# Kernel optimization log

Hardware: AMD Instinct MI355X
Metric: run time of the kernel (lower is better)

Reference implementation:

```python
import jax, jax.numpy as jnp
import numpy as np

N, G, F, H, P, OUT = 100000, 64, 64, 128, 2, 2
E = 1_600_000
BN_EPS = 1e-5  # PyG BatchNorm eps; eval mode with running_mean=0, running_var=1


def setup_inputs() -> dict:
    key = jax.random.key(0)
    ks = iter(jax.random.split(key, 64))

    def lin(din, dout):
        w = jax.random.normal(next(ks), (din, dout), jnp.float32) / np.sqrt(din).astype(np.float32)
        return w, jnp.zeros((dout,), jnp.float32)

    inp = {}
    inp["x"] = jax.random.normal(next(ks), (N, F), jnp.float32)
    inp["pos"] = jax.random.normal(next(ks), (N, P), jnp.float32)
    inp["edge_index"] = jax.random.randint(next(ks), (2, E), 0, N, dtype=jnp.int64) if jax.config.jax_enable_x64 else jax.random.randint(next(ks), (2, E), 0, N)
    inp["batch"] = jnp.sort(jax.random.randint(next(ks), (N,), 0, G))
    dims = [F + P, H + P, H + P]
    for l, din in enumerate(dims):
        w1, b1 = lin(din, H)
        w2, b2 = lin(H, H)
        inp[f"w{l}1"], inp[f"b{l}1"] = w1, b1
        inp[f"g{l}1"], inp[f"be{l}1"] = jnp.ones((H,), jnp.float32), jnp.zeros((H,), jnp.float32)
        inp[f"w{l}2"], inp[f"b{l}2"] = w2, b2
        inp[f"g{l}2"], inp[f"be{l}2"] = jnp.ones((H,), jnp.float32), jnp.zeros((H,), jnp.float32)
    inp["wlin"], inp["blin"] = lin(H, OUT)
    return inp


def _bn(h, g, b):
    # eval-mode BatchNorm with running_mean=0, running_var=1
    return h * (g * (1.0 / np.sqrt(1.0 + BN_EPS)).astype(np.float32)) + b


def _mlp(h, w1, b1, g1, be1, w2, b2, g2, be2):
    h = jax.nn.relu(_bn(h @ w1 + b1, g1, be1))
    return jax.nn.relu(_bn(h @ w2 + b2, g2, be2))


def _gin_max(x, src, dst, mlp_params):
    # GINConv with aggr='max', eps=0: mlp(x + max_{j in N(i)} x_j), empty neighborhoods -> 0 (PyG scatter fill)
    agg = jax.ops.segment_max(x[src], dst, num_segments=N)  # [N, C]
    agg = jnp.where(jnp.isneginf(agg), jnp.zeros((), agg.dtype), agg)
    return _mlp(x + agg, *mlp_params)


def reference(x, pos, edge_index, batch,
              w01, b01, g01, be01, w02, b02, g02, be02,
              w11, b11, g11, be11, w12, b12, g12, be12,
              w21, b21, g21, be21, w22, b22, g22, be22,
              wlin, blin):
    src, dst = edge_index[0], edge_index[1]
    h = jnp.concatenate([x, pos], axis=-1)                        # [N, F+P]
    h = _gin_max(h, src, dst, (w01, b01, g01, be01, w02, b02, g02, be02))
    h = jnp.concatenate([h, pos], axis=-1)                        # [N, H+P]
    h = _gin_max(h, src, dst, (w11, b11, g11, be11, w12, b12, g12, be12))
    h = jnp.concatenate([h, pos], axis=-1)
    h = _gin_max(h, src, dst, (w21, b21, g21, be21, w22, b22, g22, be22))
    pooled = jax.ops.segment_max(h, batch, num_segments=G)        # global_max_pool -> [G, H]
    pooled = jnp.where(jnp.isneginf(pooled), jnp.zeros((), pooled.dtype), pooled)
    return pooled @ wlin + blin                                   # logits [G, OUT]
```

## Files before the change

kernel.cpp:

```cpp
#include <hip/hip_runtime.h>
#include <hip/hip_fp16.h>
#include <math.h>
#include <string.h>

constexpr int HDIM = 128;
constexpr int RB   = 136;
constexpr int ZS   = 168;
constexpr float BN_INV = 0.99999500003749980f;

typedef _Float16 half8v __attribute__((ext_vector_type(8)));
typedef __attribute__((ext_vector_type(4))) float float4v;

__device__ __forceinline__ unsigned pkmax(unsigned a, unsigned b) {
  unsigned r;
  asm volatile("v_pk_max_f16 %0, %1, %2" : "=v"(r) : "v"(a), "v"(b));
  return r;
}
__device__ __forceinline__ unsigned pkadd(unsigned a, unsigned b) {
  unsigned r;
  asm volatile("v_pk_add_f16 %0, %1, %2" : "=v"(r) : "v"(a), "v"(b));
  return r;
}

__device__ __forceinline__ float us2f(unsigned short u) { __half h; memcpy(&h, &u, 2); return __half2float(h); }
__device__ __forceinline__ unsigned short f2us(float f) {
  __half h = __float2half(f); unsigned short u; memcpy(&u, &h, 2); return u;
}

__device__ __forceinline__ unsigned encf(float f) {
  unsigned u = __float_as_uint(f);
  return (u & 0x80000000u) ? ~u : (u | 0x80000000u);
}
__device__ __forceinline__ float decf(unsigned u) {
  return (u & 0x80000000u) ? __uint_as_float(u ^ 0x80000000u) : __uint_as_float(~u);
}

__global__ __launch_bounds__(256) void k_bscan(
    const int* __restrict__ bcnt, int* __restrict__ bbase, int* __restrict__ gcur,
    int nbkt, int E) {
  __shared__ int s[256];
  int tid = threadIdx.x;
  int v = (tid < nbkt) ? bcnt[tid] : 0;
  s[tid] = v;
  __syncthreads();
  for (int off = 1; off < 256; off <<= 1) {
    int t = (tid >= off) ? s[tid - off] : 0;
    __syncthreads();
    s[tid] += t;
    __syncthreads();
  }
  if (tid < nbkt) {
    int e = s[tid] - v;
    bbase[tid] = e;
    gcur[tid] = e;
  }
  if (tid == 0) bbase[nbkt] = E;
}

__global__ __launch_bounds__(256) void k_bscatter(
    const int* __restrict__ ei, int* __restrict__ gcur,
    unsigned long long* __restrict__ sorted, int E, int shift, int nbkt) {
  __shared__ int hcnt[256];
  __shared__ int hstart[256];
  __shared__ int gbase[256];
  __shared__ unsigned long long sbuf[4096];

  const int tid = threadIdx.x;
  const int base = blockIdx.x * 4096;
  const int validCount = min(4096, E - base);

  hcnt[tid] = 0;
  __syncthreads();

  int sArr[16], dArr[16];
#pragma unroll
  for (int k = 0; k < 16; ++k) {
    int e = base + k * 256 + tid;
    if (e < E) {
      sArr[k] = ei[e];
      dArr[k] = ei[E + e];
      atomicAdd(&hcnt[dArr[k] >> shift], 1);
    } else {
      sArr[k] = -1; dArr[k] = -1;
    }
  }
  __syncthreads();

  {
    int v = hcnt[tid];
    __shared__ int sc[256];
    sc[tid] = v;
    __syncthreads();
    for (int off = 1; off < 256; off <<= 1) {
      int t = (tid >= off) ? sc[tid - off] : 0;
      __syncthreads();
      sc[tid] += t;
      __syncthreads();
    }
    hstart[tid] = sc[tid] - v;
    if (tid < nbkt && v > 0) gbase[tid] = atomicAdd(&gcur[tid], v);
    hcnt[tid] = sc[tid] - v;
  }
  __syncthreads();

#pragma unroll
  for (int k = 0; k < 16; ++k) {
    if (dArr[k] >= 0) {
      int b = dArr[k] >> shift;
      int p = atomicAdd(&hcnt[b], 1);
      sbuf[p] = ((unsigned long long)(unsigned)dArr[k] << 32) | (unsigned)sArr[k];
    }
  }
  __syncthreads();

  for (int p = tid; p < validCount; p += 256) {
    unsigned long long v = sbuf[p];
    int b = (int)(v >> 32) >> shift;
    sorted[(size_t)gbase[b] + (p - hstart[b])] = v;
  }
}

__global__ __launch_bounds__(256) void k_bcsr(
    const unsigned long long* __restrict__ sorted, const int* __restrict__ bbase,
    int* __restrict__ rowptr, int* __restrict__ eidx,
    int shift, int nbkt, int N, int E) {
  __shared__ int cnt[512];
  __shared__ int excl[512];
  __shared__ int sc[256];
  const int b = blockIdx.x, tid = threadIdx.x;
  const int nodeBase = b << shift;
  const int nodesHere = min(512, N - nodeBase);
  const int lo = bbase[b], hi = bbase[b + 1];

  cnt[tid] = 0; cnt[tid + 256] = 0;
  __syncthreads();
  for (int i = lo + tid; i < hi; i += 256) {
    int d = (int)(sorted[i] >> 32);
    atomicAdd(&cnt[d - nodeBase], 1);
  }
  __syncthreads();
  int a0 = cnt[2 * tid], a1 = cnt[2 * tid + 1];
  int pv = a0 + a1;
  sc[tid] = pv;
  __syncthreads();
  for (int off = 1; off < 256; off <<= 1) {
    int t = (tid >= off) ? sc[tid - off] : 0;
    __syncthreads();
    sc[tid] += t;
    __syncthreads();
  }
  int pe = sc[tid] - pv;
  excl[2 * tid] = pe;
  excl[2 * tid + 1] = pe + a0;
  __syncthreads();
  for (int i = tid; i < 512; i += 256) {
    if (i < nodesHere) rowptr[nodeBase + i] = lo + excl[i];
    cnt[i] = excl[i];
  }
  if (b == nbkt - 1 && tid == 0) rowptr[N] = E;
  __syncthreads();
  for (int i = lo + tid; i < hi; i += 256) {
    unsigned long long v = sorted[i];
    int d = (int)(v >> 32);
    int s = (int)(v & 0xFFFFFFFFu);
    int p = atomicAdd(&cnt[d - nodeBase], 1);
    eidx[lo + p] = s;
  }
}

struct PrepArgs {
  const float *x, *pos;
  const float *w01, *w11, *w21, *w02, *w12, *w22;
  const float *b01, *g01, *e01, *b02, *g02, *e02;
  const float *b11, *g11, *e11, *b12, *g12, *e12;
  const float *b21, *g21, *e21, *b22, *g22, *e22;
  const int *ei;
  int *bcnt;
  unsigned short *h0;
  unsigned short *Wt;
  unsigned *pooled;
  float *Ep;
  int N, GH, E, shift, nbkt, chunks;
};

__global__ __launch_bounds__(256) void k_prep(PrepArgs a) {
  __shared__ int hb[256];
  const int tid = threadIdx.x;
  const int gtid = blockIdx.x * 256 + tid;

  if (blockIdx.x < a.chunks) {
    hb[tid] = 0;
    __syncthreads();
    const int base = blockIdx.x * 4096;
#pragma unroll
    for (int k = 0; k < 16; ++k) {
      int e = base + k * 256 + tid;
      if (e < a.E) atomicAdd(&hb[a.ei[a.E + e] >> a.shift], 1);
    }
    __syncthreads();
    if (tid < a.nbkt && hb[tid] > 0) atomicAdd(&a.bcnt[tid], hb[tid]);
  }

  if (gtid < a.GH) a.pooled[gtid] = 0x007FFFFFu;

  if (gtid < 61440) {
    int l = gtid / 20480, rem = gtid % 20480;
    int n = rem / 160, k = rem % 160;
    const float* W = (l == 0) ? a.w01 : ((l == 1) ? a.w11 : a.w21);
    int K = (l == 0) ? 66 : 130;
    float v = (k < K) ? W[(size_t)k * 128 + n] : 0.0f;
    a.Wt[gtid] = f2us(v);
  } else if (gtid < 110592) {
    int idx2 = gtid - 61440;
    int l = idx2 / 16384, rem = idx2 % 16384;
    int n = rem / 128, k = rem % 128;
    const float* W = (l == 0) ? a.w02 : ((l == 1) ? a.w12 : a.w22);
    a.Wt[gtid] = f2us(W[(size_t)k * 128 + n]);
  } else if (gtid < 110592 + 768) {
    int idx = gtid - 110592;
    int col = idx & 127, stage = (idx >> 7) & 1, l = idx >> 8;
    const float *bb, *gg, *ee;
    if (l == 0)      { if (!stage) { bb = a.b01; gg = a.g01; ee = a.e01; } else { bb = a.b02; gg = a.g02; ee = a.e02; } }
    else if (l == 1) { if (!stage) { bb = a.b11; gg = a.g11; ee = a.e11; } else { bb = a.b12; gg = a.g12; ee = a.e12; } }
    else             { if (!stage) { bb = a.b21; gg = a.g21; ee = a.e21; } else { bb = a.b22; gg = a.g22; ee = a.e22; } }
    float s = gg[col] * BN_INV;
    a.Ep[l * 512 + stage * 256 + col] = s;
    a.Ep[l * 512 + stage * 256 + 128 + col] = bb[col] * s + ee[col];
  }

  int r = gtid >> 6;
  if (r < a.N) {
    int lane = gtid & 63;
    a.h0[(size_t)r * RB + lane] = f2us(a.x[(size_t)r * 64 + lane]);
    float pv = (lane < 2) ? a.pos[(size_t)r * 2 + lane] : 0.0f;
    a.h0[(size_t)r * RB + 64 + lane] = f2us(pv);
    if (lane < 8) {
      a.h0[(size_t)r * RB + 128 + lane] = f2us((lane < 2) ? a.pos[(size_t)r * 2 + lane] : 0.0f);
    }
  }
}

__global__ __launch_bounds__(256) void k_agg(
    const unsigned short* __restrict__ hcat, const int* __restrict__ rowptr,
    const int* __restrict__ eidx, unsigned short* __restrict__ z,
    int actA, int doTail, int N) {
  int wid = (int)((blockIdx.x * 256 + threadIdx.x) >> 6);
  if (wid >= N) return;
  const int lane = threadIdx.x & 63;
  const int half = lane >> 5;
  const int lc = lane & 31;
  const bool act = (lc < actA) || (doTail && lc == 16);
  const int cb = lc * 8;

  const unsigned NEGINF = 0xFC00FC00u;
  unsigned m0 = NEGINF, m1 = NEGINF, m2 = NEGINF, m3 = NEGINF;

  int r0 = rowptr[wid], r1 = rowptr[wid + 1];
  int e = r0 + half;
  for (; e + 6 < r1; e += 8) {
    int s0 = eidx[e], s1 = eidx[e + 2], s2 = eidx[e + 4], s3 = eidx[e + 6];
    if (act) {
      uint4 v0 = *(const uint4*)(hcat + (size_t)s0 * RB + cb);
      uint4 v1 = *(const uint4*)(hcat + (size_t)s1 * RB + cb);
      uint4 v2 = *(const uint4*)(hcat + (size_t)s2 * RB + cb);
      uint4 v3 = *(const uint4*)(hcat + (size_t)s3 * RB + cb);
      m0 = pkmax(m0, pkmax(pkmax(v0.x, v1.x), pkmax(v2.x, v3.x)));
      m1 = pkmax(m1, pkmax(pkmax(v0.y, v1.y), pkmax(v2.y, v3.y)));
      m2 = pkmax(m2, pkmax(pkmax(v0.z, v1.z), pkmax(v2.z, v3.z)));
      m3 = pkmax(m3, pkmax(pkmax(v0.w, v1.w), pkmax(v2.w, v3.w)));
    }
  }
  for (; e < r1; e += 2) {
    int s = eidx[e];
    if (act) {
      uint4 va = *(const uint4*)(hcat + (size_t)s * RB + cb);
      m0 = pkmax(m0, va.x);
      m1 = pkmax(m1, va.y);
      m2 = pkmax(m2, va.z);
      m3 = pkmax(m3, va.w);
    }
  }

  m0 = pkmax(m0, (unsigned)__shfl_xor((int)m0, 32));
  m1 = pkmax(m1, (unsigned)__shfl_xor((int)m1, 32));
  m2 = pkmax(m2, (unsigned)__shfl_xor((int)m2, 32));
  m3 = pkmax(m3, (unsigned)__shfl_xor((int)m3, 32));

  if (half == 0 && act) {
    if (r0 == r1) { m0 = 0u; m1 = 0u; m2 = 0u; m3 = 0u; }
    uint4 sv = *(const uint4*)(hcat + (size_t)wid * RB + cb);
    uint4 o;
    o.x = pkadd(sv.x, m0);
    o.y = pkadd(sv.y, m1);
    o.z = pkadd(sv.z, m2);
    o.w = pkadd(sv.w, m3);
    *(uint4*)(z + (size_t)wid * RB + cb) = o;
  }
}

__global__ __launch_bounds__(256) void k_mlp(
    const unsigned short* __restrict__ z, int kc1, int ntot, int nreal,
    const unsigned short* __restrict__ Wt1, const float* __restrict__ Ep1,
    const unsigned short* __restrict__ Wt2, const float* __restrict__ Ep2,
    unsigned short* __restrict__ out, int N) {
  __shared__ __align__(16) unsigned short zs[4][16][ZS];
  const int tid = threadIdx.x;
  const int w = tid >> 6, lane = tid & 63;
  const int arow = lane & 15;
  const int grp  = lane >> 4;
  const int row0 = blockIdx.x * 64 + w * 16;

  for (int c = lane; c < 16 * ntot; c += 64) {
    int r = c / ntot, seg = c - r * ntot;
    uint4 v = make_uint4(0u, 0u, 0u, 0u);
    if (seg < nreal) {
      int gr = row0 + r;
      if (gr >= N) gr = N - 1;
      v = *(const uint4*)(z + (size_t)gr * RB + seg * 8);
    }
    *(uint4*)(&zs[w][r][seg * 8]) = v;
  }

  float4v acc[8];
#pragma unroll
  for (int i = 0; i < 8; ++i) acc[i] = (float4v){0.f, 0.f, 0.f, 0.f};

  for (int kc = 0; kc < kc1; ++kc) {
    half8v a = *(const half8v*)(&zs[w][arow][kc * 32 + grp * 8]);
    const unsigned short* wp = Wt1 + (size_t)arow * 160 + kc * 32 + grp * 8;
#pragma unroll
    for (int nt = 0; nt < 8; ++nt) {
      half8v b = *(const half8v*)(wp + (size_t)(nt * 16) * 160);
      acc[nt] = __builtin_amdgcn_mfma_f32_16x16x32_f16(a, b, acc[nt], 0, 0, 0);
    }
  }

#pragma unroll
  for (int nt = 0; nt < 8; ++nt) {
    int col = nt * 16 + arow;
    float sc = Ep1[col];
    float cc = Ep1[128 + col];
#pragma unroll
    for (int j = 0; j < 4; ++j) {
      float v = fmaxf(fmaf(acc[nt][j], sc, cc), 0.0f);
      zs[w][grp * 4 + j][col] = f2us(v);
    }
  }

#pragma unroll
  for (int i = 0; i < 8; ++i) acc[i] = (float4v){0.f, 0.f, 0.f, 0.f};
  for (int kc = 0; kc < 4; ++kc) {
    half8v a = *(const half8v*)(&zs[w][arow][kc * 32 + grp * 8]);
    const unsigned short* wp = Wt2 + (size_t)arow * HDIM + kc * 32 + grp * 8;
#pragma unroll
    for (int nt = 0; nt < 8; ++nt) {
      half8v b = *(const half8v*)(wp + (size_t)(nt * 16) * HDIM);
      acc[nt] = __builtin_amdgcn_mfma_f32_16x16x32_f16(a, b, acc[nt], 0, 0, 0);
    }
  }

#pragma unroll
  for (int nt = 0; nt < 8; ++nt) {
    int col = nt * 16 + arow;
    float sc = Ep2[col];
    float cc = Ep2[128 + col];
#pragma unroll
    for (int j = 0; j < 4; ++j) {
      float v = fmaxf(fmaf(acc[nt][j], sc, cc), 0.0f);
      zs[w][grp * 4 + j][col] = f2us(v);
    }
  }
  for (int c = lane; c < 16 * 16; c += 64) {
    int r = c >> 4, seg = c & 15;
    int gr = row0 + r;
    if (gr < N) {
      *(uint4*)(out + (size_t)gr * RB + seg * 8) = *(const uint4*)(&zs[w][r][seg * 8]);
    }
  }
}

__global__ __launch_bounds__(128) void k_pool(
    const unsigned short* __restrict__ hcat, const int* __restrict__ batch,
    unsigned* __restrict__ pooled, int N) {
  int base = blockIdx.x * 128;
  int c = threadIdx.x;
  int end = min(base + 128, N);
  int curg = -1;
  float m = -INFINITY;
  for (int i = base; i < end; ++i) {
    int g = batch[i];
    if (g != curg) {
      if (curg >= 0) atomicMax(&pooled[curg * HDIM + c], encf(m));
      curg = g;
      m = -INFINITY;
    }
    m = fmaxf(m, us2f(hcat[(size_t)i * RB + c]));
  }
  if (curg >= 0) atomicMax(&pooled[curg * HDIM + c], encf(m));
}

__global__ __launch_bounds__(64) void k_final(
    const unsigned* __restrict__ pooled, const float* __restrict__ wlin,
    const float* __restrict__ blin, float* __restrict__ out) {
  int g = blockIdx.x;
  int lane = threadIdx.x;
  float v0 = decf(pooled[g * HDIM + lane]);
  float v1 = decf(pooled[g * HDIM + 64 + lane]);
  if (v0 == -INFINITY) v0 = 0.0f;
  if (v1 == -INFINITY) v1 = 0.0f;
  float p0 = v0 * wlin[lane * 2 + 0] + v1 * wlin[(64 + lane) * 2 + 0];
  float p1 = v0 * wlin[lane * 2 + 1] + v1 * wlin[(64 + lane) * 2 + 1];
  for (int off = 32; off > 0; off >>= 1) {
    p0 += __shfl_down(p0, off);
    p1 += __shfl_down(p1, off);
  }
  if (lane == 0) {
    out[g * 2 + 0] = p0 + blin[0];
    out[g * 2 + 1] = p1 + blin[1];
  }
}

static inline size_t ws_align(size_t x) { return (x + 511) & ~(size_t)511; }

extern "C" void kernel_launch(void* const* d_in, const int* in_sizes, int n_in,
                              void* d_out, int out_size, void* d_ws, size_t ws_size,
                              hipStream_t stream) {
  const float* x     = (const float*)d_in[0];
  const float* pos   = (const float*)d_in[1];
  const int*   ei    = (const int*)d_in[2];
  const int*   batch = (const int*)d_in[3];
  const float* wlin  = (const float*)d_in[28];
  const float* blin  = (const float*)d_in[29];

  const int N = in_sizes[3];
  const int E = in_sizes[2] / 2;
  const int G = out_size / 2;

  int shift = 9;
  while ((((N - 1) >> shift) + 1) > 256) ++shift;
  const int nbkt = ((N - 1) >> shift) + 1;
  const int chunks = (E + 4095) / 4096;

  char* w = (char*)d_ws;
  size_t off = 0;
  auto take = [&](size_t bytes) { void* p = w + off; off += ws_align(bytes); return p; };
  int*            rowptr = (int*)take((size_t)(N + 1) * 4);
  int*            bcnt   = (int*)take(1024);
  int*            bbase  = (int*)take(2048);
  int*            gcur   = (int*)take(1024);
  int*            eidx   = (int*)take((size_t)E * 4);
  unsigned long long* sorted = (unsigned long long*)take((size_t)E * 8);
  unsigned short* hcat   = (unsigned short*)take((size_t)N * RB * 2 + 1024);
  unsigned short* z      = (unsigned short*)take((size_t)N * RB * 2 + 1024);
  unsigned short* Wt     = (unsigned short*)take((size_t)110592 * 2);
  float*          Ep     = (float*)take(3 * 2 * 2 * 128 * 4);
  unsigned*       pooled = (unsigned*)take((size_t)G * HDIM * 4);
  (void)ws_size;

  hipMemsetAsync(bcnt, 0, 1024, stream);
  {
    PrepArgs a;
    a.x = x; a.pos = pos;
    a.w01 = (const float*)d_in[4];  a.w11 = (const float*)d_in[12]; a.w21 = (const float*)d_in[20];
    a.w02 = (const float*)d_in[8];  a.w12 = (const float*)d_in[16]; a.w22 = (const float*)d_in[24];
    a.b01 = (const float*)d_in[5];  a.g01 = (const float*)d_in[6];  a.e01 = (const float*)d_in[7];
    a.b02 = (const float*)d_in[9];  a.g02 = (const float*)d_in[10]; a.e02 = (const float*)d_in[11];
    a.b11 = (const float*)d_in[13]; a.g11 = (const float*)d_in[14]; a.e11 = (const float*)d_in[15];
    a.b12 = (const float*)d_in[17]; a.g12 = (const float*)d_in[18]; a.e12 = (const float*)d_in[19];
    a.b21 = (const float*)d_in[21]; a.g21 = (const float*)d_in[22]; a.e21 = (const float*)d_in[23];
    a.b22 = (const float*)d_in[25]; a.g22 = (const float*)d_in[26]; a.e22 = (const float*)d_in[27];
    a.ei = ei; a.bcnt = bcnt;
    a.h0 = hcat; a.Wt = Wt; a.pooled = pooled; a.Ep = Ep;
    a.N = N; a.GH = G * HDIM; a.E = E; a.shift = shift; a.nbkt = nbkt; a.chunks = chunks;
    k_prep<<<(N + 3) / 4, 256, 0, stream>>>(a);
  }

  k_bscan<<<1, 256, 0, stream>>>(bcnt, bbase, gcur, nbkt, E);
  k_bscatter<<<chunks, 256, 0, stream>>>(ei, gcur, sorted, E, shift, nbkt);
  k_bcsr<<<nbkt, 256, 0, stream>>>(sorted, bbase, rowptr, eidx, shift, nbkt, N, E);

  const int actA[3]   = {9, 16, 16};
  const int doTail[3] = {0, 1, 0};
  const int kc1a[3]   = {3, 5, 5};
  const int ntotA[3]  = {12, 21, 21};
  const int nrealA[3] = {12, 17, 17};
  const int aggBlocks = (N + 3) / 4;
  const int mlpBlocks = (N + 63) / 64;

  for (int l = 0; l < 3; ++l) {
    const unsigned short* Wt1 = Wt + (size_t)l * 20480;
    const unsigned short* Wt2 = Wt + 61440 + (size_t)l * 16384;
    const float* Ep1 = Ep + l * 512;
    const float* Ep2 = Ep + l * 512 + 256;

    k_agg<<<aggBlocks, 256, 0, stream>>>(hcat, rowptr, eidx, z, actA[l], doTail[l], N);
    k_mlp<<<mlpBlocks, 256, 0, stream>>>(z, kc1a[l], ntotA[l], nrealA[l],
                                         Wt1, Ep1, Wt2, Ep2, hcat, N);
  }

  k_pool<<<(N + 127) / 128, 128, 0, stream>>>(hcat, batch, pooled, N);
  k_final<<<G, 64, 0, stream>>>(pooled, wlin, blin, (float*)d_out);
}
```

Before: 494.7 us.

## Fuse global max pool into last MLP and swizzle blocks across XCDs

The last layer's MLP kernel now does the per-graph max pooling straight from its shared-memory output tile with atomics, so it no longer writes hcat and the separate pool kernel is gone. Both agg and mlp kernels also remap block IDs so consecutive blocks land on the same XCD, aiming for better L2 locality of neighbouring rows. The pool step now runs with one block per 64 rows instead of per 128 rows, which roughly doubles the atomics. The remapping also depends on how the hardware assigns blocks to XCDs.

```diff
diff --git a/kernel.cpp b/kernel.cpp
--- a/kernel.cpp
+++ b/kernel.cpp
@@ -33,6 +33,13 @@
 }
 __device__ __forceinline__ float decf(unsigned u) {
   return (u & 0x80000000u) ? __uint_as_float(u ^ 0x80000000u) : __uint_as_float(~u);
+}
+
+__device__ __forceinline__ int xcd_swz(int bid, int nwg) {
+  int q = nwg >> 3, r = nwg & 7;
+  int xcd = bid & 7, idx = bid >> 3;
+  int base = (xcd < r) ? xcd * (q + 1) : r * (q + 1) + (xcd - r) * q;
+  return base + idx;
 }
 
 __global__ __launch_bounds__(256) void k_bscan(
@@ -243,8 +250,9 @@
 __global__ __launch_bounds__(256) void k_agg(
     const unsigned short* __restrict__ hcat, const int* __restrict__ rowptr,
     const int* __restrict__ eidx, unsigned short* __restrict__ z,
-    int actA, int doTail, int N) {
-  int wid = (int)((blockIdx.x * 256 + threadIdx.x) >> 6);
+    int actA, int doTail, int N, int nwg) {
+  const int blk = xcd_swz(blockIdx.x, nwg);
+  int wid = (int)((blk * 256 + threadIdx.x) >> 6);
   if (wid >= N) return;
   const int lane = threadIdx.x & 63;
   const int half = lane >> 5;
@@ -302,13 +310,17 @@
     const unsigned short* __restrict__ z, int kc1, int ntot, int nreal,
     const unsigned short* __restrict__ Wt1, const float* __restrict__ Ep1,
     const unsigned short* __restrict__ Wt2, const float* __restrict__ Ep2,
-    unsigned short* __restrict__ out, int N) {
+    unsigned short* __restrict__ out, const int* __restrict__ batch,
+    unsigned* __restrict__ pooled, int doPool, int N, int nwg) {
   __shared__ __align__(16) unsigned short zs[4][16][ZS];
+  __shared__ int bid_s[64];
   const int tid = threadIdx.x;
+  const int blk = xcd_swz(blockIdx.x, nwg);
   const int w = tid >> 6, lane = tid & 63;
   const int arow = lane & 15;
   const int grp  = lane >> 4;
-  const int row0 = blockIdx.x * 64 + w * 16;
+  const int brow0 = blk * 64;
+  const int row0 = brow0 + w * 16;
 
   for (int c = lane; c < 16 * ntot; c += 64) {
     int r = c / ntot, seg = c - r * ntot;
@@ -370,33 +382,39 @@
       zs[w][grp * 4 + j][col] = f2us(v);
     }
   }
-  for (int c = lane; c < 16 * 16; c += 64) {
-    int r = c >> 4, seg = c & 15;
-    int gr = row0 + r;
-    if (gr < N) {
-      *(uint4*)(out + (size_t)gr * RB + seg * 8) = *(const uint4*)(&zs[w][r][seg * 8]);
-    }
-  }
-}
-
-__global__ __launch_bounds__(128) void k_pool(
-    const unsigned short* __restrict__ hcat, const int* __restrict__ batch,
-    unsigned* __restrict__ pooled, int N) {
-  int base = blockIdx.x * 128;
-  int c = threadIdx.x;
-  int end = min(base + 128, N);
-  int curg = -1;
-  float m = -INFINITY;
-  for (int i = base; i < end; ++i) {
-    int g = batch[i];
-    if (g != curg) {
+
+  if (!doPool) {
+    for (int c = lane; c < 16 * 16; c += 64) {
+      int r = c >> 4, seg = c & 15;
+      int gr = row0 + r;
+      if (gr < N) {
+        *(uint4*)(out + (size_t)gr * RB + seg * 8) = *(const uint4*)(&zs[w][r][seg * 8]);
+      }
+    }
+  } else {
+    __syncthreads();
+    if (tid < 64) {
+      int gr = brow0 + tid;
+      bid_s[tid] = (gr < N) ? batch[gr] : -1;
+    }
+    __syncthreads();
+    if (tid < 128) {
+      const int c = tid;
+      int curg = -1;
+      float m = -INFINITY;
+      for (int r = 0; r < 64; ++r) {
+        int g = bid_s[r];
+        if (g < 0) break;
+        if (g != curg) {
+          if (curg >= 0) atomicMax(&pooled[curg * HDIM + c], encf(m));
+          curg = g;
+          m = -INFINITY;
+        }
+        m = fmaxf(m, us2f(zs[r >> 4][r & 15][c]));
+      }
       if (curg >= 0) atomicMax(&pooled[curg * HDIM + c], encf(m));
-      curg = g;
-      m = -INFINITY;
-    }
-    m = fmaxf(m, us2f(hcat[(size_t)i * RB + c]));
-  }
-  if (curg >= 0) atomicMax(&pooled[curg * HDIM + c], encf(m));
+    }
+  }
 }
 
 __global__ __launch_bounds__(64) void k_final(
@@ -493,11 +511,12 @@
     const float* Ep1 = Ep + l * 512;
     const float* Ep2 = Ep + l * 512 + 256;
 
-    k_agg<<<aggBlocks, 256, 0, stream>>>(hcat, rowptr, eidx, z, actA[l], doTail[l], N);
+    k_agg<<<aggBlocks, 256, 0, stream>>>(hcat, rowptr, eidx, z, actA[l], doTail[l],
+                                         N, aggBlocks);
     k_mlp<<<mlpBlocks, 256, 0, stream>>>(z, kc1a[l], ntotA[l], nrealA[l],
-                                         Wt1, Ep1, Wt2, Ep2, hcat, N);
-  }
-
-  k_pool<<<(N + 127) / 128, 128, 0, stream>>>(hcat, batch, pooled, N);
+                                         Wt1, Ep1, Wt2, Ep2, hcat, batch, pooled,
+                                         (l == 2) ? 1 : 0, N, mlpBlocks);
+  }
+
   k_final<<<G, 64, 0, stream>>>(pooled, wlin, blin, (float*)d_out);
 }
```

New measurement: 458.9 us. 1.08x faster.
